# Optimization experiments

Hardware: AMD Instinct MI355X
Metric: run time of the kernel (lower is better)

## Reference

```python
import jax, jax.numpy as jnp
import numpy as np

B, D, UNITS = 32768, 1024, 1024
NB_FACTOR, SPARSITY = 3, 32
NB = D // SPARSITY  # 32 blocks of 32x32 per block-diagonal factor


def _block_t_matmul(kb, y):
    # kb: [nb, bi, bo] block-diagonal factor values; y: [nb*bi, batch]
    # computes blockdiag(kb)^T @ y without materializing the dense matrix
    nb, bi, bo = kb.shape
    yb = y.reshape(nb, bi, -1)                      # [nb, bi, batch]
    out = jnp.einsum('nio,nib->nob', kb, yb)        # [nb, bo, batch]
    return out.reshape(nb * bo, -1)


def setup_inputs() -> dict:
    key = jax.random.key(0)
    ks = jax.random.split(key, 9)
    return {
        'x': jax.random.normal(ks[0], (B, D), jnp.float32),
        'P0': jax.random.normal(ks[1], (D, D), jnp.float32),
        'P1': jax.random.normal(ks[2], (D, D), jnp.float32),
        'P2': jax.random.normal(ks[3], (D, D), jnp.float32),
        'P3': jax.random.normal(ks[4], (UNITS, UNITS), jnp.float32),
        'K0': jax.random.normal(ks[5], (NB, SPARSITY, SPARSITY), jnp.float32) * 0.05,
        'K1': jax.random.normal(ks[6], (NB, SPARSITY, SPARSITY), jnp.float32) * 0.05,
        'K2': jax.random.normal(ks[7], (NB, SPARSITY, SPARSITY), jnp.float32) * 0.05,
        'bias': jax.random.normal(ks[8], (UNITS,), jnp.float32),
    }


def reference(x, P0, P1, P2, P3, K0, K1, K2, bias):
    # output = (softmax(P3) @ Bd2^T @ softmax(P2) @ Bd1^T @ softmax(P1) @ Bd0^T @ softmax(P0) @ x^T)^T + bias
    y = x.T                                          # [D, B]
    y = jax.nn.softmax(P0, axis=1) @ y
    for kb, perm in ((K0, P1), (K1, P2), (K2, P3)):
        y = _block_t_matmul(kb, y)
        y = jax.nn.softmax(perm, axis=1) @ y
    out = y.T + bias                                 # [B, UNITS]
    return out
```

## Files before the change

### kernel.cpp

```cpp
#include <hip/hip_runtime.h>
#include <hip/hip_bf16.h>

typedef __bf16 bf16x8 __attribute__((ext_vector_type(8)));
typedef float f32x4 __attribute__((ext_vector_type(4)));
typedef unsigned short u16x8 __attribute__((ext_vector_type(8)));

__device__ __forceinline__ unsigned short f2bf(float f) {
  unsigned u = __float_as_uint(f);
  u += 0x7FFF + ((u >> 16) & 1);
  return (unsigned short)(u >> 16);
}
__device__ __forceinline__ float bf2f(unsigned short h) {
  return __uint_as_float((unsigned)h << 16);
}

__device__ __forceinline__ void gload_lds16(const void* g, void* l) {
  __builtin_amdgcn_global_load_lds(
      (const __attribute__((address_space(1))) void*)g,
      (__attribute__((address_space(3))) void*)l, 16, 0, 0);
}

__device__ __forceinline__ void convert_slice(const float* __restrict__ x,
                                              unsigned short* __restrict__ xb,
                                              int base8, int cnt8, int cb, int nb)
{
  int i = cb * 256 + (int)threadIdx.x;
  const int stride = nb * 256;
  for (; i < cnt8; i += stride) {
    const size_t g = (size_t)(base8 + i);
    float4 v0 = ((const float4*)x)[2 * g];
    float4 v1 = ((const float4*)x)[2 * g + 1];
    u16x8 uv;
    uv[0] = f2bf(v0.x); uv[1] = f2bf(v0.y); uv[2] = f2bf(v0.z); uv[3] = f2bf(v0.w);
    uv[4] = f2bf(v1.x); uv[5] = f2bf(v1.y); uv[6] = f2bf(v1.z); uv[7] = f2bf(v1.w);
    ((u16x8*)xb)[g] = uv;
  }
}

__global__ __launch_bounds__(256)
void softmax4_kernel(const float* __restrict__ P0, const float* __restrict__ P1,
                     const float* __restrict__ P2, const float* __restrict__ P3,
                     unsigned short* __restrict__ S,
                     const float* __restrict__ cvx, unsigned short* __restrict__ cvxb,
                     int cvt_cnt)
{
  if (blockIdx.x >= 4096) {
    convert_slice(cvx, cvxb, 0, cvt_cnt, blockIdx.x - 4096, gridDim.x - 4096);
    return;
  }
  const int bid = blockIdx.x;
  const int mat = bid >> 10, row = bid & 1023;
  const float* P = (mat == 0 ? P0 : mat == 1 ? P1 : mat == 2 ? P2 : P3) + (size_t)row * 1024;
  unsigned short* out = S + ((size_t)mat << 20) + (size_t)row * 1024;
  const int t = threadIdx.x, w = t >> 6, l = t & 63;
  float4 v = ((const float4*)P)[t];
  float mx = fmaxf(fmaxf(v.x, v.y), fmaxf(v.z, v.w));
  #pragma unroll
  for (int off = 32; off > 0; off >>= 1) mx = fmaxf(mx, __shfl_xor(mx, off));
  __shared__ float redA[4], redB[4];
  if (l == 0) redA[w] = mx;
  __syncthreads();
  mx = fmaxf(fmaxf(redA[0], redA[1]), fmaxf(redA[2], redA[3]));
  float e0 = __expf(v.x - mx), e1 = __expf(v.y - mx);
  float e2 = __expf(v.z - mx), e3 = __expf(v.w - mx);
  float s = e0 + e1 + e2 + e3;
  #pragma unroll
  for (int off = 32; off > 0; off >>= 1) s += __shfl_xor(s, off);
  if (l == 0) redB[w] = s;
  __syncthreads();
  s = redB[0] + redB[1] + redB[2] + redB[3];
  float inv = 1.0f / s;
  ushort4 o;
  o.x = f2bf(e0 * inv); o.y = f2bf(e1 * inv);
  o.z = f2bf(e2 * inv); o.w = f2bf(e3 * inv);
  ((ushort4*)out)[t] = o;
}

__device__ __forceinline__ void bdT_body(const float* __restrict__ Kb,
                                         const unsigned short* __restrict__ in,
                                         unsigned short* __restrict__ outT, int bid)
{
  const int n = bid >> 2;
  const int c = (bid & 3) * 256 + threadIdx.x;
  __shared__ float Ks[32][33];
  for (int t = threadIdx.x; t < 1024; t += 256)
    Ks[t >> 5][t & 31] = Kb[n * 1024 + t];
  __syncthreads();
  float ri[32];
  #pragma unroll
  for (int i = 0; i < 32; ++i)
    ri[i] = bf2f(in[(size_t)(n * 32 + i) * 1024 + c]);
  unsigned short ov[32];
  #pragma unroll
  for (int o = 0; o < 32; ++o) {
    float acc = 0.f;
    #pragma unroll
    for (int i = 0; i < 32; ++i) acc = fmaf(Ks[i][o], ri[i], acc);
    ov[o] = f2bf(acc);
  }
  u16x8* dst = (u16x8*)(outT + (size_t)c * 1024 + n * 32);
  const u16x8* src = (const u16x8*)ov;
  #pragma unroll
  for (int q = 0; q < 4; ++q) dst[q] = src[q];
}

__global__ __launch_bounds__(256)
void blockdiagT_dual_kernel(const float* Ka, const unsigned short* ina, unsigned short* outa,
                            const float* Kb2, const unsigned short* inb, unsigned short* outb,
                            const float* cvx, unsigned short* cvxb, int cvt_base, int cvt_cnt)
{
  const int bid = blockIdx.x;
  if (bid >= 256) {
    convert_slice(cvx, cvxb, cvt_base, cvt_cnt, bid - 256, gridDim.x - 256);
    return;
  }
  const bool sec = bid >= 128;
  bdT_body(sec ? Kb2 : Ka, sec ? inb : ina, sec ? outb : outa, sec ? bid - 128 : bid);
}

template<int TILE, bool A_FP32, bool OUT_BIAS, bool RBD>
__device__ __forceinline__ void gemm_body(const void* __restrict__ Av,
                                          const unsigned short* __restrict__ B,
                                          void* __restrict__ Cv, const float* __restrict__ bias,
                                          int N, int K, int nprim, int bid,
                                          const float* __restrict__ KR)
{
  constexpr int FR  = TILE / 32;
  constexpr int SIT = TILE / 32;
  __shared__ unsigned short Asm[TILE * 64];
  __shared__ unsigned short Bsm[TILE * 64];
  const int tid = threadIdx.x;
  const int w = tid >> 6, l = tid & 63;
  const int cpx = nprim >> 3;
  const int swz = (bid & 7) * cpx + (bid >> 3);
  const int ntn = N / TILE;
  const int n0 = (swz % ntn) * TILE;
  const int m0 = (swz / ntn) * TILE;
  const int wr = (w >> 1) * (TILE / 2), wc = (w & 1) * (TILE / 2);
  const int lr = l & 15, kg = (l >> 4) << 3;

  f32x4 acc[FR][FR] = {};
  const int KT = K >> 6;
  for (int kt = 0; kt < KT; ++kt) {
    const int k0 = kt << 6;
    if (kt) __syncthreads();
    #pragma unroll
    for (int it = 0; it < SIT; ++it) {
      int li = it * 256 + tid;
      int row = li >> 3, c8 = (li & 7) << 3;
      const unsigned short* g = B + (size_t)(n0 + row) * K + (k0 + c8);
      gload_lds16(g, (char*)Bsm + it * 4096 + w * 1024);
    }
    if (A_FP32) {
      const float* Af = (const float*)Av;
      #pragma unroll
      for (int p = 0; p < SIT; ++p) {
        int row = (tid >> 3) + p * 32;
        int c8 = (tid & 7) << 3;
        const float* g = Af + (size_t)(m0 + row) * K + (k0 + c8);
        float4 v0 = ((const float4*)g)[0];
        float4 v1 = ((const float4*)g)[1];
        u16x8 uv;
        uv[0] = f2bf(v0.x); uv[1] = f2bf(v0.y); uv[2] = f2bf(v0.z); uv[3] = f2bf(v0.w);
        uv[4] = f2bf(v1.x); uv[5] = f2bf(v1.y); uv[6] = f2bf(v1.z); uv[7] = f2bf(v1.w);
        *(u16x8*)&Asm[row * 64 + c8] = uv;
      }
    } else {
      const unsigned short* Ab = (const unsigned short*)Av;
      #pragma unroll
      for (int it = 0; it < SIT; ++it) {
        int li = it * 256 + tid;
        int row = li >> 3, c8 = (li & 7) << 3;
        const unsigned short* g = Ab + (size_t)(m0 + row) * K + (k0 + c8);
        gload_lds16(g, (char*)Asm + it * 4096 + w * 1024);
      }
    }
    __syncthreads();
    #pragma unroll
    for (int ks = 0; ks < 2; ++ks) {
      const int kb = ks * 32 + kg;
      bf16x8 af[FR], bfr[FR];
      #pragma unroll
      for (int i = 0; i < FR; ++i)
        af[i] = *(const bf16x8*)&Asm[(wr + i * 16 + lr) * 64 + kb];
      #pragma unroll
      for (int j = 0; j < FR; ++j)
        bfr[j] = *(const bf16x8*)&Bsm[(wc + j * 16 + lr) * 64 + kb];
      #pragma unroll
      for (int i = 0; i < FR; ++i)
        #pragma unroll
        for (int j = 0; j < FR; ++j)
          acc[i][j] = __builtin_amdgcn_mfma_f32_16x16x32_bf16(af[i], bfr[j], acc[i][j], 0, 0, 0);
    }
  }
  const int cr = (l >> 4) << 2;
  const int cc = l & 15;
  if (RBD) {
    __shared__ float tileS[64][65];
    __shared__ float Kt[2][32][33];
    __syncthreads();
    #pragma unroll
    for (int j = 0; j < FR; ++j)
      #pragma unroll
      for (int i = 0; i < FR; ++i)
        #pragma unroll
        for (int r = 0; r < 4; ++r)
          tileS[wr + i * 16 + cr + r][wc + j * 16 + cc] = acc[i][j][r];
    for (int idx = tid; idx < 2048; idx += 256) {
      int blk = idx >> 10, rem = idx & 1023;
      Kt[blk][rem >> 5][rem & 31] = KR[(size_t)((n0 >> 5) + blk) * 1024 + rem];
    }
    __syncthreads();
    const int row = tid & 63, cq = (tid >> 6) << 4;
    const int nb2 = cq >> 5, co = cq & 31;
    float av[16] = {};
    #pragma unroll 4
    for (int o = 0; o < 32; ++o) {
      float a = tileS[row][nb2 * 32 + o];
      #pragma unroll
      for (int ii = 0; ii < 16; ++ii)
        av[ii] = fmaf(a, Kt[nb2][o][co + ii], av[ii]);
    }
    u16x8 ov[2];
    #pragma unroll
    for (int ii = 0; ii < 16; ++ii) ov[ii >> 3][ii & 7] = f2bf(av[ii]);
    unsigned short* Cz = (unsigned short*)Cv;
    u16x8* dst = (u16x8*)&Cz[(size_t)(m0 + row) * N + n0 + cq];
    dst[0] = ov[0]; dst[1] = ov[1];
  } else if (OUT_BIAS) {
    float* C = (float*)Cv;
    #pragma unroll
    for (int j = 0; j < FR; ++j) {
      int col = n0 + wc + j * 16 + cc;
      float bv = bias[col];
      #pragma unroll
      for (int i = 0; i < FR; ++i) {
        int rbase = m0 + wr + i * 16 + cr;
        #pragma unroll
        for (int r = 0; r < 4; ++r)
          C[(size_t)(rbase + r) * N + col] = acc[i][j][r] + bv;
      }
    }
  } else {
    unsigned short* C = (unsigned short*)Cv;
    #pragma unroll
    for (int j = 0; j < FR; ++j) {
      int col = n0 + wc + j * 16 + cc;
      #pragma unroll
      for (int i = 0; i < FR; ++i) {
        int rbase = m0 + wr + i * 16 + cr;
        #pragma unroll
        for (int r = 0; r < 4; ++r)
          C[(size_t)(rbase + r) * N + col] = f2bf(acc[i][j][r]);
      }
    }
  }
}

template<int TILE, bool A_FP32, bool OUT_BIAS>
__global__ __launch_bounds__(256)
void gemm_bt_kernel(const void* __restrict__ Av, const unsigned short* __restrict__ B,
                    void* __restrict__ Cv, const float* __restrict__ bias,
                    int N, int K, int nprim,
                    const float* cvx, unsigned short* cvxb, int cvt_base, int cvt_cnt)
{
  if ((int)blockIdx.x >= nprim) {
    convert_slice(cvx, cvxb, cvt_base, cvt_cnt, blockIdx.x - nprim, gridDim.x - nprim);
    return;
  }
  gemm_body<TILE, A_FP32, OUT_BIAS, false>(Av, B, Cv, bias, N, K, nprim, blockIdx.x, nullptr);
}

__global__ __launch_bounds__(256)
void gemm_dual_kernel(const unsigned short* A0, const unsigned short* B0, unsigned short* C0,
                      const unsigned short* A1, const unsigned short* B1, unsigned short* C1,
                      const float* KR,
                      const float* cvx, unsigned short* cvxb, int cvt_base, int cvt_cnt)
{
  const int bid = blockIdx.x;
  if (bid >= 512) {
    convert_slice(cvx, cvxb, cvt_base, cvt_cnt, bid - 512, gridDim.x - 512);
    return;
  }
  if (bid < 256)
    gemm_body<64, false, false, false>(A0, B0, (void*)C0, nullptr, 1024, 1024, 256, bid, nullptr);
  else
    gemm_body<64, false, false, true>(A1, B1, (void*)C1, nullptr, 1024, 1024, 256, bid - 256, KR);
}

__global__ __launch_bounds__(512, 2)
void gemm256_kernel(const unsigned short* __restrict__ A,
                    const unsigned short* __restrict__ B,
                    float* __restrict__ C, const float* __restrict__ bias,
                    int N, int K)
{
  extern __shared__ __align__(16) char lds[];
  const int tid = threadIdx.x;
  const int w = tid >> 6, l = tid & 63;
  const int wm = w >> 2, wn = w & 3;
  const int lr = l & 15;
  const int klo = (l >> 4) << 4;
  const int sw  = (lr & 7) << 4;

  const int nwg = gridDim.x;
  const int bid = blockIdx.x;
  const int cpx = nwg >> 3;
  const int swz = (bid & 7) * cpx + (bid >> 3);
  const int ntn = N >> 8;
  const int n0 = (swz % ntn) << 8;
  const int m0 = (swz / ntn) << 8;

  unsigned int aoff[2][2], boff[2][2];
  #pragma unroll
  for (int q = 0; q < 2; ++q)
    #pragma unroll
    for (int it = 0; it < 2; ++it) {
      int L = it * 8192 + tid * 16;
      int r = L >> 7;
      int cs = (L & 127) ^ ((r & 7) << 4);
      aoff[q][it] = (unsigned)(m0 + q * 128 + r) * K + (cs >> 1);
      boff[q][it] = (unsigned)(n0 + q * 128 + r) * K + (cs >> 1);
    }
  char* ldsA = lds;
  char* ldsB = lds + 65536;
  const int wdst = w * 1024;

#define STG_A(bufo, q, k0) do { \
    gload_lds16(A + aoff[q][0] + (k0), ldsA + (bufo) + (q) * 16384 + wdst); \
    gload_lds16(A + aoff[q][1] + (k0), ldsA + (bufo) + (q) * 16384 + 8192 + wdst); } while (0)
#define STG_B(bufo, q, k0) do { \
    gload_lds16(B + boff[q][0] + (k0), ldsB + (bufo) + (q) * 16384 + wdst); \
    gload_lds16(B + boff[q][1] + (k0), ldsB + (bufo) + (q) * 16384 + 8192 + wdst); } while (0)

  f32x4 acc[2][2][4][2] = {};

  STG_A(0, 0, 0); STG_B(0, 0, 0); STG_B(0, 1, 0); STG_A(0, 1, 0);

  const int NT = K >> 6;
  int curo = 0;
  for (int t = 0; t < NT; ++t) {
    const int nxto = curo ^ 32768;
    const int k1 = (t + 1) << 6;
    asm volatile("s_waitcnt vmcnt(0)" ::: "memory");
    __builtin_amdgcn_s_barrier();
    if (t + 1 < NT) { STG_A(nxto, 0, k1); STG_B(nxto, 0, k1); STG_B(nxto, 1, k1); STG_A(nxto, 1, k1); }
    const char* Ab = ldsA + curo;
    const char* Bb = ldsB + curo;
    bf16x8 av[2][2][4];
    bf16x8 bvr[2][2][2];
    #pragma unroll
    for (int ks = 0; ks < 2; ++ks) {
      const int cb = (ks * 64 + klo) ^ sw;
      #pragma unroll
      for (int qi = 0; qi < 2; ++qi)
        #pragma unroll
        for (int i = 0; i < 4; ++i)
          av[ks][qi][i] = *(const bf16x8*)(Ab + qi * 16384 + (wm * 64 + i * 16 + lr) * 128 + cb);
      #pragma unroll
      for (int qj = 0; qj < 2; ++qj)
        #pragma unroll
        for (int j = 0; j < 2; ++j)
          bvr[ks][qj][j] = *(const bf16x8*)(Bb + qj * 16384 + (wn * 32 + j * 16 + lr) * 128 + cb);
    }
    __builtin_amdgcn_s_setprio(1);
    #pragma unroll
    for (int ks = 0; ks < 2; ++ks)
      #pragma unroll
      for (int qi = 0; qi < 2; ++qi)
        #pragma unroll
        for (int i = 0; i < 4; ++i)
          #pragma unroll
          for (int qj = 0; qj < 2; ++qj)
            #pragma unroll
            for (int j = 0; j < 2; ++j)
              acc[qi][qj][i][j] = __builtin_amdgcn_mfma_f32_16x16x32_bf16(
                  av[ks][qi][i], bvr[ks][qj][j], acc[qi][qj][i][j], 0, 0, 0);
    __builtin_amdgcn_s_setprio(0);
    curo = nxto;
  }

  const int cr = (l >> 4) << 2;
  const int cc = l & 15;
  #pragma unroll
  for (int qi = 0; qi < 2; ++qi)
    #pragma unroll
    for (int qj = 0; qj < 2; ++qj)
      #pragma unroll
      for (int j = 0; j < 2; ++j) {
        const int col = n0 + qj * 128 + wn * 32 + j * 16 + cc;
        const float bvv = bias[col];
        #pragma unroll
        for (int i = 0; i < 4; ++i) {
          const int rbase = m0 + qi * 128 + wm * 64 + i * 16 + cr;
          #pragma unroll
          for (int r = 0; r < 4; ++r)
            C[(size_t)(rbase + r) * N + col] = acc[qi][qj][i][j][r] + bvv;
        }
      }
#undef STG_A
#undef STG_B
}

extern "C" void kernel_launch(void* const* d_in, const int* in_sizes, int n_in,
                              void* d_out, int out_size, void* d_ws, size_t ws_size,
                              hipStream_t stream) {
  (void)in_sizes; (void)n_in; (void)out_size;
  const float* x    = (const float*)d_in[0];
  const float* P0   = (const float*)d_in[1];
  const float* P1   = (const float*)d_in[2];
  const float* P2   = (const float*)d_in[3];
  const float* P3   = (const float*)d_in[4];
  const float* K0   = (const float*)d_in[5];
  const float* K1   = (const float*)d_in[6];
  const float* K2   = (const float*)d_in[7];
  const float* bias = (const float*)d_in[8];

  unsigned short* S  = (unsigned short*)d_ws;
  unsigned short* s0 = S;
  unsigned short* s1 = S + (1u << 20);
  unsigned short* s2 = S + (2u << 20);
  unsigned short* s3 = S + (3u << 20);
  unsigned short* t0 = S + (4u << 20);
  unsigned short* t1 = S + (5u << 20);
  unsigned short* Xb = S + (6u << 20);
  const size_t need = ((size_t)6 * (1u << 20) + (size_t)32768 * 1024) * 2;
  const bool have_xb = ws_size >= need;
  unsigned short* xbp = have_xb ? Xb : nullptr;

  const int SL = 524288;
  const int cvt2 = have_xb ? 2 * SL : 0;
  const int tail_smx = have_xb ? 1024 : 0;
  const int tail_512 = have_xb ? 512 : 0;

  softmax4_kernel<<<4096 + tail_smx, 256, 0, stream>>>(P0, P1, P2, P3, S, x, xbp, cvt2);

  blockdiagT_dual_kernel<<<256 + tail_512, 256, 0, stream>>>(K2, s2, t0, K0, s0, t1,
                                                             x, xbp, 2 * SL, cvt2);

  gemm_dual_kernel<<<512 + tail_512, 256, 0, stream>>>(s3, t0, s0, t1, s1, s2, K1,
                                                       x, xbp, 4 * SL, cvt2);

  gemm_bt_kernel<64, false, false><<<256 + tail_512, 256, 0, stream>>>((const void*)s0, s2,
      (void*)t0, nullptr, 1024, 1024, 256, x, xbp, 6 * SL, cvt2);

  bool ok256 = false;
  if (have_xb) {
    hipError_t e = hipFuncSetAttribute((const void*)gemm256_kernel,
                                       hipFuncAttributeMaxDynamicSharedMemorySize, 131072);
    ok256 = (e == hipSuccess);
  }
  if (ok256) {
    gemm256_kernel<<<512, 512, 131072, stream>>>(Xb, t0, (float*)d_out, bias, 1024, 1024);
  } else if (have_xb) {
    gemm_bt_kernel<128, false, true><<<2048, 256, 0, stream>>>((const void*)Xb, t0,
        d_out, bias, 1024, 1024, 2048, nullptr, nullptr, 0, 0);
  } else {
    gemm_bt_kernel<128, true, true><<<2048, 256, 0, stream>>>((const void*)x, t0,
        d_out, bias, 1024, 1024, 2048, nullptr, nullptr, 0, 0);
  }
}
```

Measured before the change: 158.4 us.

## Fuse fp32-to-bf16 conversion of x into final GEMM A-tile staging

Removes the separate conversion of x to bf16, which was spread as tail blocks across the earlier kernels. The final 256x256 GEMM now loads fp32 x rows into registers, converts them to bf16, and writes them into swizzled LDS after the MFMA phase, prefetching one tile ahead. This drops the 64MB bf16 workspace write and re-read plus the side work in the small kernels. The cost is register-staged A loads that replace asynchronous global-to-LDS loads, twice the A bytes per tile read from global memory, and conversion ALU work inside the GEMM loop.

```diff
diff --git a/kernel.cpp b/kernel.cpp
--- a/kernel.cpp
+++ b/kernel.cpp
@@ -20,34 +20,11 @@
       (__attribute__((address_space(3))) void*)l, 16, 0, 0);
 }
 
-__device__ __forceinline__ void convert_slice(const float* __restrict__ x,
-                                              unsigned short* __restrict__ xb,
-                                              int base8, int cnt8, int cb, int nb)
-{
-  int i = cb * 256 + (int)threadIdx.x;
-  const int stride = nb * 256;
-  for (; i < cnt8; i += stride) {
-    const size_t g = (size_t)(base8 + i);
-    float4 v0 = ((const float4*)x)[2 * g];
-    float4 v1 = ((const float4*)x)[2 * g + 1];
-    u16x8 uv;
-    uv[0] = f2bf(v0.x); uv[1] = f2bf(v0.y); uv[2] = f2bf(v0.z); uv[3] = f2bf(v0.w);
-    uv[4] = f2bf(v1.x); uv[5] = f2bf(v1.y); uv[6] = f2bf(v1.z); uv[7] = f2bf(v1.w);
-    ((u16x8*)xb)[g] = uv;
-  }
-}
-
 __global__ __launch_bounds__(256)
 void softmax4_kernel(const float* __restrict__ P0, const float* __restrict__ P1,
                      const float* __restrict__ P2, const float* __restrict__ P3,
-                     unsigned short* __restrict__ S,
-                     const float* __restrict__ cvx, unsigned short* __restrict__ cvxb,
-                     int cvt_cnt)
-{
-  if (blockIdx.x >= 4096) {
-    convert_slice(cvx, cvxb, 0, cvt_cnt, blockIdx.x - 4096, gridDim.x - 4096);
-    return;
-  }
+                     unsigned short* __restrict__ S)
+{
   const int bid = blockIdx.x;
   const int mat = bid >> 10, row = bid & 1023;
   const float* P = (mat == 0 ? P0 : mat == 1 ? P1 : mat == 2 ? P2 : P3) + (size_t)row * 1024;
@@ -106,14 +83,9 @@
 
 __global__ __launch_bounds__(256)
 void blockdiagT_dual_kernel(const float* Ka, const unsigned short* ina, unsigned short* outa,
-                            const float* Kb2, const unsigned short* inb, unsigned short* outb,
-                            const float* cvx, unsigned short* cvxb, int cvt_base, int cvt_cnt)
+                            const float* Kb2, const unsigned short* inb, unsigned short* outb)
 {
   const int bid = blockIdx.x;
-  if (bid >= 256) {
-    convert_slice(cvx, cvxb, cvt_base, cvt_cnt, bid - 256, gridDim.x - 256);
-    return;
-  }
   const bool sec = bid >= 128;
   bdT_body(sec ? Kb2 : Ka, sec ? inb : ina, sec ? outb : outa, sec ? bid - 128 : bid);
 }
@@ -261,27 +233,17 @@
 __global__ __launch_bounds__(256)
 void gemm_bt_kernel(const void* __restrict__ Av, const unsigned short* __restrict__ B,
                     void* __restrict__ Cv, const float* __restrict__ bias,
-                    int N, int K, int nprim,
-                    const float* cvx, unsigned short* cvxb, int cvt_base, int cvt_cnt)
-{
-  if ((int)blockIdx.x >= nprim) {
-    convert_slice(cvx, cvxb, cvt_base, cvt_cnt, blockIdx.x - nprim, gridDim.x - nprim);
-    return;
-  }
+                    int N, int K, int nprim)
+{
   gemm_body<TILE, A_FP32, OUT_BIAS, false>(Av, B, Cv, bias, N, K, nprim, blockIdx.x, nullptr);
 }
 
 __global__ __launch_bounds__(256)
 void gemm_dual_kernel(const unsigned short* A0, const unsigned short* B0, unsigned short* C0,
                       const unsigned short* A1, const unsigned short* B1, unsigned short* C1,
-                      const float* KR,
-                      const float* cvx, unsigned short* cvxb, int cvt_base, int cvt_cnt)
+                      const float* KR)
 {
   const int bid = blockIdx.x;
-  if (bid >= 512) {
-    convert_slice(cvx, cvxb, cvt_base, cvt_cnt, bid - 512, gridDim.x - 512);
-    return;
-  }
   if (bid < 256)
     gemm_body<64, false, false, false>(A0, B0, (void*)C0, nullptr, 1024, 1024, 256, bid, nullptr);
   else
@@ -289,7 +251,7 @@
 }
 
 __global__ __launch_bounds__(512, 2)
-void gemm256_kernel(const unsigned short* __restrict__ A,
+void gemm256_kernel(const float* __restrict__ A,
                     const unsigned short* __restrict__ B,
                     float* __restrict__ C, const float* __restrict__ bias,
                     int N, int K)
@@ -310,7 +272,7 @@
   const int n0 = (swz % ntn) << 8;
   const int m0 = (swz / ntn) << 8;
 
-  unsigned int aoff[2][2], boff[2][2];
+  unsigned int boff[2][2];
   #pragma unroll
   for (int q = 0; q < 2; ++q)
     #pragma unroll
@@ -318,36 +280,49 @@
       int L = it * 8192 + tid * 16;
       int r = L >> 7;
       int cs = (L & 127) ^ ((r & 7) << 4);
-      aoff[q][it] = (unsigned)(m0 + q * 128 + r) * K + (cs >> 1);
       boff[q][it] = (unsigned)(n0 + q * 128 + r) * K + (cs >> 1);
     }
+  const int arow = tid >> 3;
+  const int acol = (tid & 7) << 3;
   char* ldsA = lds;
   char* ldsB = lds + 65536;
   const int wdst = w * 1024;
 
-#define STG_A(bufo, q, k0) do { \
-    gload_lds16(A + aoff[q][0] + (k0), ldsA + (bufo) + (q) * 16384 + wdst); \
-    gload_lds16(A + aoff[q][1] + (k0), ldsA + (bufo) + (q) * 16384 + 8192 + wdst); } while (0)
 #define STG_B(bufo, q, k0) do { \
     gload_lds16(B + boff[q][0] + (k0), ldsB + (bufo) + (q) * 16384 + wdst); \
     gload_lds16(B + boff[q][1] + (k0), ldsB + (bufo) + (q) * 16384 + 8192 + wdst); } while (0)
+#define A_LOAD(k0) do { \
+    _Pragma("unroll") for (int p = 0; p < 4; ++p) { \
+      const float* g = A + (size_t)(m0 + p * 64 + arow) * K + (k0) + acol; \
+      sa0[p] = ((const float4*)g)[0]; sa1[p] = ((const float4*)g)[1]; } } while (0)
+#define A_WRITE(bufo) do { \
+    _Pragma("unroll") for (int p = 0; p < 4; ++p) { \
+      const int row = p * 64 + arow; \
+      u16x8 uv; \
+      uv[0] = f2bf(sa0[p].x); uv[1] = f2bf(sa0[p].y); uv[2] = f2bf(sa0[p].z); uv[3] = f2bf(sa0[p].w); \
+      uv[4] = f2bf(sa1[p].x); uv[5] = f2bf(sa1[p].y); uv[6] = f2bf(sa1[p].z); uv[7] = f2bf(sa1[p].w); \
+      *(u16x8*)(ldsA + (bufo) + ((row >> 7) << 14) + ((row & 127) << 7) \
+                + (((acol << 1)) ^ ((row & 7) << 4))) = uv; } } while (0)
 
   f32x4 acc[2][2][4][2] = {};
-
-  STG_A(0, 0, 0); STG_B(0, 0, 0); STG_B(0, 1, 0); STG_A(0, 1, 0);
+  float4 sa0[4], sa1[4];
+
+  STG_B(0, 0, 0); STG_B(0, 1, 0);
+  A_LOAD(0); A_WRITE(0);
 
   const int NT = K >> 6;
   int curo = 0;
   for (int t = 0; t < NT; ++t) {
     const int nxto = curo ^ 32768;
     const int k1 = (t + 1) << 6;
-    asm volatile("s_waitcnt vmcnt(0)" ::: "memory");
+    asm volatile("s_waitcnt vmcnt(0) lgkmcnt(0)" ::: "memory");
     __builtin_amdgcn_s_barrier();
-    if (t + 1 < NT) { STG_A(nxto, 0, k1); STG_B(nxto, 0, k1); STG_B(nxto, 1, k1); STG_A(nxto, 1, k1); }
+    const bool st = (t + 1 < NT);
+    if (st) { STG_B(nxto, 0, k1); STG_B(nxto, 1, k1); A_LOAD(k1); }
     const char* Ab = ldsA + curo;
     const char* Bb = ldsB + curo;
-    bf16x8 av[2][2][4];
-    bf16x8 bvr[2][2][2];
+    bf16x8 fa[2][2][4];
+    bf16x8 fb[2][2][2];
     #pragma unroll
     for (int ks = 0; ks < 2; ++ks) {
       const int cb = (ks * 64 + klo) ^ sw;
@@ -355,12 +330,12 @@
       for (int qi = 0; qi < 2; ++qi)
         #pragma unroll
         for (int i = 0; i < 4; ++i)
-          av[ks][qi][i] = *(const bf16x8*)(Ab + qi * 16384 + (wm * 64 + i * 16 + lr) * 128 + cb);
+          fa[ks][qi][i] = *(const bf16x8*)(Ab + qi * 16384 + (wm * 64 + i * 16 + lr) * 128 + cb);
       #pragma unroll
       for (int qj = 0; qj < 2; ++qj)
         #pragma unroll
         for (int j = 0; j < 2; ++j)
-          bvr[ks][qj][j] = *(const bf16x8*)(Bb + qj * 16384 + (wn * 32 + j * 16 + lr) * 128 + cb);
+          fb[ks][qj][j] = *(const bf16x8*)(Bb + qj * 16384 + (wn * 32 + j * 16 + lr) * 128 + cb);
     }
     __builtin_amdgcn_s_setprio(1);
     #pragma unroll
@@ -374,8 +349,9 @@
             #pragma unroll
             for (int j = 0; j < 2; ++j)
               acc[qi][qj][i][j] = __builtin_amdgcn_mfma_f32_16x16x32_bf16(
-                  av[ks][qi][i], bvr[ks][qj][j], acc[qi][qj][i][j], 0, 0, 0);
+                  fa[ks][qi][i], fb[ks][qj][j], acc[qi][qj][i][j], 0, 0, 0);
     __builtin_amdgcn_s_setprio(0);
+    if (st) A_WRITE(nxto);
     curo = nxto;
   }
 
@@ -397,8 +373,9 @@
             C[(size_t)(rbase + r) * N + col] = acc[qi][qj][i][j][r] + bvv;
         }
       }
-#undef STG_A
 #undef STG_B
+#undef A_LOAD
+#undef A_WRITE
 }
 
 extern "C" void kernel_launch(void* const* d_in, const int* in_sizes, int n_in,
@@ -422,40 +399,26 @@
   unsigned short* s3 = S + (3u << 20);
   unsigned short* t0 = S + (4u << 20);
   unsigned short* t1 = S + (5u << 20);
-  unsigned short* Xb = S + (6u << 20);
-  const size_t need = ((size_t)6 * (1u << 20) + (size_t)32768 * 1024) * 2;
-  const bool have_xb = ws_size >= need;
-  unsigned short* xbp = have_xb ? Xb : nullptr;
-
-  const int SL = 524288;
-  const int cvt2 = have_xb ? 2 * SL : 0;
-  const int tail_smx = have_xb ? 1024 : 0;
-  const int tail_512 = have_xb ? 512 : 0;
-
-  softmax4_kernel<<<4096 + tail_smx, 256, 0, stream>>>(P0, P1, P2, P3, S, x, xbp, cvt2);
-
-  blockdiagT_dual_kernel<<<256 + tail_512, 256, 0, stream>>>(K2, s2, t0, K0, s0, t1,
-                                                             x, xbp, 2 * SL, cvt2);
-
-  gemm_dual_kernel<<<512 + tail_512, 256, 0, stream>>>(s3, t0, s0, t1, s1, s2, K1,
-                                                       x, xbp, 4 * SL, cvt2);
-
-  gemm_bt_kernel<64, false, false><<<256 + tail_512, 256, 0, stream>>>((const void*)s0, s2,
-      (void*)t0, nullptr, 1024, 1024, 256, x, xbp, 6 * SL, cvt2);
+
+  softmax4_kernel<<<4096, 256, 0, stream>>>(P0, P1, P2, P3, S);
+
+  blockdiagT_dual_kernel<<<256, 256, 0, stream>>>(K2, s2, t0, K0, s0, t1);
+
+  gemm_dual_kernel<<<512, 256, 0, stream>>>(s3, t0, s0, t1, s1, s2, K1);
+
+  gemm_bt_kernel<64, false, false><<<256, 256, 0, stream>>>((const void*)s0, s2,
+      (void*)t0, nullptr, 1024, 1024, 256);
 
   bool ok256 = false;
-  if (have_xb) {
+  {
     hipError_t e = hipFuncSetAttribute((const void*)gemm256_kernel,
                                        hipFuncAttributeMaxDynamicSharedMemorySize, 131072);
     ok256 = (e == hipSuccess);
   }
   if (ok256) {
-    gemm256_kernel<<<512, 512, 131072, stream>>>(Xb, t0, (float*)d_out, bias, 1024, 1024);
-  } else if (have_xb) {
-    gemm_bt_kernel<128, false, true><<<2048, 256, 0, stream>>>((const void*)Xb, t0,
-        d_out, bias, 1024, 1024, 2048, nullptr, nullptr, 0, 0);
+    gemm256_kernel<<<512, 512, 131072, stream>>>(x, t0, (float*)d_out, bias, 1024, 1024);
   } else {
     gemm_bt_kernel<128, true, true><<<2048, 256, 0, stream>>>((const void*)x, t0,
-        d_out, bias, 1024, 1024, 2048, nullptr, nullptr, 0, 0);
-  }
-}
+        d_out, bias, 1024, 1024, 2048);
+  }
+}
```

Measured after the change: 308.3 us. 1.95x slower.

## Process two M tiles per workgroup in final GEMM and rebalance conversion slices

Applied to the files above, without the earlier changes.

The final 256x256-tile GEMM now covers two consecutive M tiles per workgroup, launching 256 instead of 512 workgroups. It keeps one pipelined loop across both tiles, writes the first tile's output mid-loop and resets the accumulators. This cuts the grid to one wave on 256 CUs, removing the second-wave tail, and keeps the shared B tile warm in cache. The x-to-bf16 conversion work is also redistributed, giving more slices to the softmax and blockdiag kernels and fewer to the later GEMMs. The risk is that the mid-loop epilogue stalls the pipeline, and that the heavier early kernels lengthen the critical path.

```diff
diff --git a/kernel.cpp b/kernel.cpp
--- a/kernel.cpp
+++ b/kernel.cpp
@@ -288,6 +288,30 @@
     gemm_body<64, false, false, true>(A1, B1, (void*)C1, nullptr, 1024, 1024, 256, bid - 256, KR);
 }
 
+__device__ __forceinline__ void write_c256(const f32x4 (&acc)[2][2][4][2],
+    float* __restrict__ C, const float* __restrict__ bias,
+    int mb, int n0, int N, int wm, int wn, int l)
+{
+  const int cr = (l >> 4) << 2;
+  const int cc = l & 15;
+  #pragma unroll
+  for (int qi = 0; qi < 2; ++qi)
+    #pragma unroll
+    for (int qj = 0; qj < 2; ++qj)
+      #pragma unroll
+      for (int j = 0; j < 2; ++j) {
+        const int col = n0 + qj * 128 + wn * 32 + j * 16 + cc;
+        const float bvv = bias[col];
+        #pragma unroll
+        for (int i = 0; i < 4; ++i) {
+          const int rbase = mb + qi * 128 + wm * 64 + i * 16 + cr;
+          #pragma unroll
+          for (int r = 0; r < 4; ++r)
+            C[(size_t)(rbase + r) * N + col] = acc[qi][qj][i][j][r] + bvv;
+        }
+      }
+}
+
 __global__ __launch_bounds__(512, 2)
 void gemm256_kernel(const unsigned short* __restrict__ A,
                     const unsigned short* __restrict__ B,
@@ -308,7 +332,7 @@
   const int swz = (bid & 7) * cpx + (bid >> 3);
   const int ntn = N >> 8;
   const int n0 = (swz % ntn) << 8;
-  const int m0 = (swz / ntn) << 8;
+  const int m0 = (swz / ntn) << 9;
 
   unsigned int aoff[2][2], boff[2][2];
   #pragma unroll
@@ -321,6 +345,7 @@
       aoff[q][it] = (unsigned)(m0 + q * 128 + r) * K + (cs >> 1);
       boff[q][it] = (unsigned)(n0 + q * 128 + r) * K + (cs >> 1);
     }
+  const int mAdv = K << 8;
   char* ldsA = lds;
   char* ldsB = lds + 65536;
   const int wdst = w * 1024;
@@ -336,14 +361,17 @@
 
   STG_A(0, 0, 0); STG_B(0, 0, 0); STG_B(0, 1, 0); STG_A(0, 1, 0);
 
-  const int NT = K >> 6;
+  const int NT  = K >> 6;
+  const int NT2 = NT << 1;
   int curo = 0;
-  for (int t = 0; t < NT; ++t) {
+  for (int t = 0; t < NT2; ++t) {
     const int nxto = curo ^ 32768;
-    const int k1 = (t + 1) << 6;
+    const int tn = t + 1;
+    const int ka = ((tn & (NT - 1)) << 6) + ((tn >= NT) ? mAdv : 0);
+    const int kb = (tn & (NT - 1)) << 6;
     asm volatile("s_waitcnt vmcnt(0)" ::: "memory");
     __builtin_amdgcn_s_barrier();
-    if (t + 1 < NT) { STG_A(nxto, 0, k1); STG_B(nxto, 0, k1); STG_B(nxto, 1, k1); STG_A(nxto, 1, k1); }
+    if (tn < NT2) { STG_A(nxto, 0, ka); STG_B(nxto, 0, kb); STG_B(nxto, 1, kb); STG_A(nxto, 1, ka); }
     const char* Ab = ldsA + curo;
     const char* Bb = ldsB + curo;
     bf16x8 av[2][2][4];
@@ -376,27 +404,23 @@
               acc[qi][qj][i][j] = __builtin_amdgcn_mfma_f32_16x16x32_bf16(
                   av[ks][qi][i], bvr[ks][qj][j], acc[qi][qj][i][j], 0, 0, 0);
     __builtin_amdgcn_s_setprio(0);
+    if (t == NT - 1) {
+      write_c256(acc, C, bias, m0, n0, N, wm, wn, l);
+      #pragma unroll
+      for (int qi = 0; qi < 2; ++qi)
+        #pragma unroll
+        for (int qj = 0; qj < 2; ++qj)
+          #pragma unroll
+          for (int i = 0; i < 4; ++i)
+            #pragma unroll
+            for (int j = 0; j < 2; ++j)
+              #pragma unroll
+              for (int r = 0; r < 4; ++r)
+                acc[qi][qj][i][j][r] = 0.f;
+    }
     curo = nxto;
   }
-
-  const int cr = (l >> 4) << 2;
-  const int cc = l & 15;
-  #pragma unroll
-  for (int qi = 0; qi < 2; ++qi)
-    #pragma unroll
-    for (int qj = 0; qj < 2; ++qj)
-      #pragma unroll
-      for (int j = 0; j < 2; ++j) {
-        const int col = n0 + qj * 128 + wn * 32 + j * 16 + cc;
-        const float bvv = bias[col];
-        #pragma unroll
-        for (int i = 0; i < 4; ++i) {
-          const int rbase = m0 + qi * 128 + wm * 64 + i * 16 + cr;
-          #pragma unroll
-          for (int r = 0; r < 4; ++r)
-            C[(size_t)(rbase + r) * N + col] = acc[qi][qj][i][j][r] + bvv;
-        }
-      }
+  write_c256(acc, C, bias, m0 + 256, n0, N, wm, wn, l);
 #undef STG_A
 #undef STG_B
 }
@@ -428,20 +452,21 @@
   unsigned short* xbp = have_xb ? Xb : nullptr;
 
   const int SL = 524288;
-  const int cvt2 = have_xb ? 2 * SL : 0;
-  const int tail_smx = have_xb ? 1024 : 0;
-  const int tail_512 = have_xb ? 512 : 0;
-
-  softmax4_kernel<<<4096 + tail_smx, 256, 0, stream>>>(P0, P1, P2, P3, S, x, xbp, cvt2);
-
-  blockdiagT_dual_kernel<<<256 + tail_512, 256, 0, stream>>>(K2, s2, t0, K0, s0, t1,
-                                                             x, xbp, 2 * SL, cvt2);
-
-  gemm_dual_kernel<<<512 + tail_512, 256, 0, stream>>>(s3, t0, s0, t1, s1, s2, K1,
-                                                       x, xbp, 4 * SL, cvt2);
-
-  gemm_bt_kernel<64, false, false><<<256 + tail_512, 256, 0, stream>>>((const void*)s0, s2,
-      (void*)t0, nullptr, 1024, 1024, 256, x, xbp, 6 * SL, cvt2);
+  const int cvt3 = have_xb ? 3 * SL : 0;
+  const int cvt1 = have_xb ? SL : 0;
+  const int tail_big = have_xb ? 2048 : 0;
+  const int tail_sm  = have_xb ? 512 : 0;
+
+  softmax4_kernel<<<4096 + tail_big, 256, 0, stream>>>(P0, P1, P2, P3, S, x, xbp, cvt3);
+
+  blockdiagT_dual_kernel<<<256 + tail_big, 256, 0, stream>>>(K2, s2, t0, K0, s0, t1,
+                                                             x, xbp, 3 * SL, cvt3);
+
+  gemm_dual_kernel<<<512 + tail_sm, 256, 0, stream>>>(s3, t0, s0, t1, s1, s2, K1,
+                                                      x, xbp, 6 * SL, cvt1);
+
+  gemm_bt_kernel<64, false, false><<<256 + tail_sm, 256, 0, stream>>>((const void*)s0, s2,
+      (void*)t0, nullptr, 1024, 1024, 256, x, xbp, 7 * SL, cvt1);
 
   bool ok256 = false;
   if (have_xb) {
@@ -450,7 +475,7 @@
     ok256 = (e == hipSuccess);
   }
   if (ok256) {
-    gemm256_kernel<<<512, 512, 131072, stream>>>(Xb, t0, (float*)d_out, bias, 1024, 1024);
+    gemm256_kernel<<<256, 512, 131072, stream>>>(Xb, t0, (float*)d_out, bias, 1024, 1024);
   } else if (have_xb) {
     gemm_bt_kernel<128, false, true><<<2048, 256, 0, stream>>>((const void*)Xb, t0,
         d_out, bias, 1024, 1024, 2048, nullptr, nullptr, 0, 0);
```

Result: slower. 233.1 us (+47.2%).
